# Kernel optimization log

Hardware: AMD Instinct MI355X
Metric: run time of the kernel (lower is better)

Reference implementation:

```python
import jax, jax.numpy as jnp
import numpy as np

NUM_LANDMARKS = 256
PINV_ITERS = 6


def iterative_inv(K):
    # Newton-Schulz iterative pseudo-inverse (Nystromformer), K: [B, m, m]
    I = jnp.eye(K.shape[-1], dtype=K.dtype)
    V = K.swapaxes(-1, -2) / (jnp.max(jnp.sum(K, axis=-2)) * jnp.max(jnp.sum(K, axis=-1)))
    for _ in range(PINV_ITERS):
        KV = K @ V
        V = 0.25 * V @ (13.0 * I - KV @ (15.0 * I - KV @ (7.0 * I - KV)))
    return V


def nystrom_attention_matrix(q, k, m):
    # q, k: [B, N, d] -> approximate softmax(q k^T / sqrt(d)) of shape [B, N, N]
    B, N, d = q.shape
    scale = 1.0 / jnp.sqrt(jnp.asarray(d, q.dtype))
    L = N // m
    q_l = q.reshape(B, m, L, d).mean(axis=2)  # landmark queries [B, m, d]
    k_l = k.reshape(B, m, L, d).mean(axis=2)  # landmark keys    [B, m, d]
    k1 = jax.nn.softmax(jnp.einsum('bnd,bmd->bnm', q, k_l) * scale, axis=-1)   # [B, N, m]
    k2 = jax.nn.softmax(jnp.einsum('bld,bmd->blm', q_l, k_l) * scale, axis=-1) # [B, m, m]
    k3 = jax.nn.softmax(jnp.einsum('bmd,bnd->bmn', q_l, k) * scale, axis=-1)   # [B, m, N]
    return (k1 @ iterative_inv(k2)) @ k3  # [B, N, N]


def setup_inputs() -> dict:
    key = jax.random.key(0)
    ks = jax.random.split(key, 8)
    B, C, T, W, H = 2, 64, 4, 32, 32
    d = C // 8
    scale = 0.05  # keep q.k scores in a sane softmax range
    return {
        'x': jax.random.normal(ks[0], (B, C, T, W, H), dtype=jnp.float32),
        'wq': jax.random.normal(ks[1], (d, C), dtype=jnp.float32) * scale,
        'bq': jax.random.normal(ks[2], (d,), dtype=jnp.float32) * scale,
        'wk': jax.random.normal(ks[3], (d, C), dtype=jnp.float32) * scale,
        'bk': jax.random.normal(ks[4], (d,), dtype=jnp.float32) * scale,
        'wv': jax.random.normal(ks[5], (C, C), dtype=jnp.float32) * scale,
        'bv': jax.random.normal(ks[6], (C,), dtype=jnp.float32) * scale,
        'gamma': jax.random.normal(ks[7], (1,), dtype=jnp.float32),
    }


def reference(x, wq, bq, wk, bk, wv, bv, gamma):
    B, C, T, W, H = x.shape
    N = T * W * H
    xf = x.reshape(B, C, N)
    # 1x1x1 Conv3d == per-token linear over channels
    q = jnp.einsum('oc,bcn->bno', wq, xf) + bq            # [B, N, C//8]
    k = jnp.einsum('oc,bcn->bno', wk, xf) + bk            # [B, N, C//8]
    v = jnp.einsum('oc,bcn->bon', wv, xf) + bv[None, :, None]  # [B, C, N]
    attn = nystrom_attention_matrix(q, k, NUM_LANDMARKS)  # [B, N, N]
    # out = bmm(value, attn^T): out[b,c,i] = sum_j v[b,c,j] * attn[b,i,j]
    out = jnp.einsum('bcj,bij->bci', v, attn).reshape(B, C, T, W, H)
    out = gamma[0] * out + x
    return out, attn
```

## Files before the change

### kernel.cpp

```cpp
#include <hip/hip_runtime.h>
#include <hip/hip_bf16.h>
#include <math.h>

#define NB 2
#define NC 64
#define ND 8
#define NN 4096
#define NM 256
#define NL 16
#define SCALE 0.35355339059327373f

typedef __attribute__((ext_vector_type(4))) float f32x4;
typedef __attribute__((ext_vector_type(8))) short bf16x8;

__device__ inline ushort f2bf(float f) {
  __hip_bfloat16 h = __float2bfloat16(f);
  return *reinterpret_cast<ushort*>(&h);
}
__device__ inline float bf2f(ushort u) {
  return __uint_as_float(((unsigned int)u) << 16);
}

__device__ inline void gl_lds16(const void* g, void* l) {
  __builtin_amdgcn_global_load_lds(
      (const __attribute__((address_space(1))) unsigned int*)g,
      (__attribute__((address_space(3))) unsigned int*)l, 16, 0, 0);
}

__global__ __launch_bounds__(256) void qkv2_kernel(
    const float* __restrict__ x,
    const float* __restrict__ wq, const float* __restrict__ bq,
    const float* __restrict__ wk, const float* __restrict__ bk,
    const float* __restrict__ wv, const float* __restrict__ bv,
    float* __restrict__ q, float* __restrict__ k, float* __restrict__ v) {
  __shared__ float ws[NC];
  int o = blockIdx.x;
  int b = blockIdx.z;
  int n0 = blockIdx.y * 1024;
  int t = threadIdx.x;
  const float* wrow;
  float bias;
  if (o < ND)            { wrow = wq + (size_t)o * NC;            bias = bq[o]; }
  else if (o < 2 * ND)   { wrow = wk + (size_t)(o - ND) * NC;     bias = bk[o - ND]; }
  else                   { wrow = wv + (size_t)(o - 2 * ND) * NC; bias = bv[o - 2 * ND]; }
  if (t < NC) ws[t] = wrow[t];
  __syncthreads();
  int n = n0 + t * 4;
  float4 acc = {bias, bias, bias, bias};
  #pragma unroll
  for (int c = 0; c < NC; ++c) {
    float wc = ws[c];
    float4 xv = *(const float4*)(x + ((size_t)b * NC + c) * NN + n);
    acc.x += wc * xv.x; acc.y += wc * xv.y; acc.z += wc * xv.z; acc.w += wc * xv.w;
  }
  if (o < ND) {
    float* qp = q + ((size_t)b * NN + n) * ND + o;
    qp[0] = acc.x; qp[8] = acc.y; qp[16] = acc.z; qp[24] = acc.w;
  } else if (o < 2 * ND) {
    float* kp = k + ((size_t)b * NN + n) * ND + (o - ND);
    kp[0] = acc.x; kp[8] = acc.y; kp[16] = acc.z; kp[24] = acc.w;
  } else {
    *(float4*)(v + ((size_t)b * NC + (o - 2 * ND)) * NN + n) = acc;
  }
}

__global__ void landmark_kernel(const float* __restrict__ q, const float* __restrict__ k,
                                float* __restrict__ ql, float* __restrict__ kl) {
  int idx = blockIdx.x * 256 + threadIdx.x;
  int b = idx / (NM * ND), r = idx % (NM * ND), i = r / ND, o = r % ND;
  float sq = 0.f, sk = 0.f;
  for (int l = 0; l < NL; ++l) {
    size_t base = ((size_t)b * NN + i * NL + l) * ND + o;
    sq += q[base]; sk += k[base];
  }
  ql[idx] = sq * (1.0f / NL);
  kl[idx] = sk * (1.0f / NL);
}

__global__ __launch_bounds__(256) void scores_softmax_m_bf16(
    const float* __restrict__ Q, int R, const float* __restrict__ KL,
    ushort* __restrict__ out) {
  __shared__ float skl[NM][9];
  int b = blockIdx.y;
  int t = threadIdx.x;
  for (int i = t; i < NM * ND; i += 256) skl[i >> 3][i & 7] = KL[(size_t)b * NM * ND + i];
  __syncthreads();
  int wave = t >> 6, lane = t & 63;
  int r = blockIdx.x * 4 + wave;
  const float* qrow = Q + ((size_t)b * R + r) * ND;
  float qr[ND];
  #pragma unroll
  for (int dd = 0; dd < ND; ++dd) qr[dd] = qrow[dd];
  float sc[4];
  float lmax = -1e30f;
  #pragma unroll
  for (int s = 0; s < 4; ++s) {
    int j = lane + 64 * s;
    float a = 0.f;
    #pragma unroll
    for (int dd = 0; dd < ND; ++dd) a += qr[dd] * skl[j][dd];
    sc[s] = a * SCALE;
    lmax = fmaxf(lmax, sc[s]);
  }
  for (int off = 32; off; off >>= 1) lmax = fmaxf(lmax, __shfl_xor(lmax, off));
  float lsum = 0.f;
  #pragma unroll
  for (int s = 0; s < 4; ++s) { sc[s] = expf(sc[s] - lmax); lsum += sc[s]; }
  for (int off = 32; off; off >>= 1) lsum += __shfl_xor(lsum, off);
  float inv = 1.0f / lsum;
  #pragma unroll
  for (int s = 0; s < 4; ++s)
    out[((size_t)b * R + r) * NM + lane + 64 * s] = f2bf(sc[s] * inv);
}

__global__ __launch_bounds__(256) void scores_softmax_m_f32(
    const float* __restrict__ Q, int R, const float* __restrict__ KL,
    float* __restrict__ out) {
  __shared__ float skl[NM][9];
  int b = blockIdx.y;
  int t = threadIdx.x;
  for (int i = t; i < NM * ND; i += 256) skl[i >> 3][i & 7] = KL[(size_t)b * NM * ND + i];
  __syncthreads();
  int wave = t >> 6, lane = t & 63;
  int r = blockIdx.x * 4 + wave;
  const float* qrow = Q + ((size_t)b * R + r) * ND;
  float qr[ND];
  #pragma unroll
  for (int dd = 0; dd < ND; ++dd) qr[dd] = qrow[dd];
  float sc[4];
  float lmax = -1e30f;
  #pragma unroll
  for (int s = 0; s < 4; ++s) {
    int j = lane + 64 * s;
    float a = 0.f;
    #pragma unroll
    for (int dd = 0; dd < ND; ++dd) a += qr[dd] * skl[j][dd];
    sc[s] = a * SCALE;
    lmax = fmaxf(lmax, sc[s]);
  }
  for (int off = 32; off; off >>= 1) lmax = fmaxf(lmax, __shfl_xor(lmax, off));
  float lsum = 0.f;
  #pragma unroll
  for (int s = 0; s < 4; ++s) { sc[s] = expf(sc[s] - lmax); lsum += sc[s]; }
  for (int off = 32; off; off >>= 1) lsum += __shfl_xor(lsum, off);
  float inv = 1.0f / lsum;
  #pragma unroll
  for (int s = 0; s < 4; ++s) out[((size_t)b * R + r) * NM + lane + 64 * s] = sc[s] * inv;
}

__global__ __launch_bounds__(256) void scores_softmax_n(
    const float* __restrict__ QL, const float* __restrict__ Kt,
    float* __restrict__ out) {
  __shared__ float wred[4], wsum[4];
  int b = blockIdx.y, i = blockIdx.x;
  int t = threadIdx.x;
  float qr[ND];
  #pragma unroll
  for (int dd = 0; dd < ND; ++dd) qr[dd] = QL[((size_t)b * NM + i) * ND + dd];
  float sc[16];
  float lmax = -1e30f;
  #pragma unroll
  for (int s = 0; s < 16; ++s) {
    int n = t + 256 * s;
    const float* kp = Kt + ((size_t)b * NN + n) * ND;
    float a = 0.f;
    #pragma unroll
    for (int dd = 0; dd < ND; ++dd) a += qr[dd] * kp[dd];
    sc[s] = a * SCALE;
    lmax = fmaxf(lmax, sc[s]);
  }
  for (int off = 32; off; off >>= 1) lmax = fmaxf(lmax, __shfl_xor(lmax, off));
  if ((t & 63) == 0) wred[t >> 6] = lmax;
  __syncthreads();
  lmax = fmaxf(fmaxf(wred[0], wred[1]), fmaxf(wred[2], wred[3]));
  float lsum = 0.f;
  #pragma unroll
  for (int s = 0; s < 16; ++s) { sc[s] = expf(sc[s] - lmax); lsum += sc[s]; }
  for (int off = 32; off; off >>= 1) lsum += __shfl_xor(lsum, off);
  if ((t & 63) == 0) wsum[t >> 6] = lsum;
  __syncthreads();
  lsum = wsum[0] + wsum[1] + wsum[2] + wsum[3];
  float inv = 1.0f / lsum;
  #pragma unroll
  for (int s = 0; s < 16; ++s) out[((size_t)b * NM + i) * NN + t + 256 * s] = sc[s] * inv;
}

__global__ __launch_bounds__(256) void denom_kernel(const float* __restrict__ k2,
                                                    float* __restrict__ denw) {
  __shared__ float red[256];
  int b = blockIdx.x;
  int t = threadIdx.x;
  float cs = 0.f;
  for (int i = 0; i < NM; ++i) cs += k2[((size_t)b * NM + i) * NM + t];
  red[t] = cs;
  __syncthreads();
  for (int off = 128; off; off >>= 1) {
    if (t < off) red[t] = fmaxf(red[t], red[t + off]);
    __syncthreads();
  }
  if (t == 0) denw[b] = red[0];
}

__global__ void vinit_kernel(const float* __restrict__ k2, const float* __restrict__ denw,
                             float* __restrict__ V) {
  int idx = blockIdx.x * 256 + threadIdx.x;
  int b = idx / (NM * NM), r = idx % (NM * NM), i = r / NM, j = r % NM;
  float dval = 1.0f / fmaxf(denw[0], denw[1]);
  V[idx] = k2[((size_t)b * NM + j) * NM + i] * dval;
}

__global__ __launch_bounds__(256) void gemm_rk32(
    const float* __restrict__ A, const float* __restrict__ Bm,
    float* __restrict__ out, float s_a, float s_ab) {
  int b = blockIdx.z;
  int bi = blockIdx.y * 32, bj = blockIdx.x * 32;
  __shared__ float As[32][260];
  __shared__ float Bs[256][36];
  int t = threadIdx.x;
  const float* Ab = A + (size_t)b * NM * NM;
  const float* Bb = Bm + (size_t)b * NM * NM;
  #pragma unroll
  for (int q = 0; q < 8; ++q) {
    int s = q * 256 + t;
    int ar = s >> 6, ac = (s & 63) * 4;
    *(float4*)&As[ar][ac] = *(const float4*)(Ab + (size_t)(bi + ar) * NM + ac);
    int br = s >> 3, bc = (s & 7) * 4;
    *(float4*)&Bs[br][bc] = *(const float4*)(Bb + (size_t)br * NM + bj + bc);
  }
  __syncthreads();
  int tx = t & 15, ty = t >> 4;
  float acc[2][2] = {};
  #pragma unroll 8
  for (int kk = 0; kk < NM; ++kk) {
    float a0 = As[ty * 2][kk], a1 = As[ty * 2 + 1][kk];
    float b0 = Bs[kk][tx * 2], b1 = Bs[kk][tx * 2 + 1];
    acc[0][0] += a0 * b0; acc[0][1] += a0 * b1;
    acc[1][0] += a1 * b0; acc[1][1] += a1 * b1;
  }
  #pragma unroll
  for (int i = 0; i < 2; ++i)
    #pragma unroll
    for (int j = 0; j < 2; ++j) {
      size_t o = ((size_t)b * NM + bi + ty * 2 + i) * NM + bj + tx * 2 + j;
      float r = s_ab * acc[i][j];
      if (s_a != 0.0f) r += s_a * A[o];
      out[o] = r;
    }
}

__global__ __launch_bounds__(256) void cvt_vinv_kernel(const float* __restrict__ Va,
                                                       ushort* __restrict__ Vt) {
  int b = blockIdx.z;
  int n0 = blockIdx.x * 32, m0 = blockIdx.y * 32;
  __shared__ float tile[32][33];
  int t = threadIdx.x;
  int r = t >> 3, c4 = (t & 7) * 4;
  float4 v = *(const float4*)(Va + ((size_t)b * NM + m0 + r) * NM + n0 + c4);
  tile[c4][r] = v.x; tile[c4 + 1][r] = v.y; tile[c4 + 2][r] = v.z; tile[c4 + 3][r] = v.w;
  __syncthreads();
  ushort4 u;
  u.x = f2bf(tile[r][c4]);     u.y = f2bf(tile[r][c4 + 1]);
  u.z = f2bf(tile[r][c4 + 2]); u.w = f2bf(tile[r][c4 + 3]);
  *(ushort4*)(Vt + ((size_t)b * NM + n0 + r) * NM + m0 + c4) = u;
}

__global__ __launch_bounds__(256) void cvt_t_kernel(const float* __restrict__ k3,
                                                    ushort* __restrict__ k3t) {
  int b = blockIdx.z;
  int n0 = blockIdx.x * 32, m0 = blockIdx.y * 32;
  __shared__ float tile[32][33];
  int t = threadIdx.x;
  int r = t >> 3, c4 = (t & 7) * 4;
  float4 v = *(const float4*)(k3 + ((size_t)b * NM + m0 + r) * NN + n0 + c4);
  tile[c4][r] = v.x; tile[c4 + 1][r] = v.y; tile[c4 + 2][r] = v.z; tile[c4 + 3][r] = v.w;
  __syncthreads();
  ushort4 u;
  u.x = f2bf(tile[r][c4]);     u.y = f2bf(tile[r][c4 + 1]);
  u.z = f2bf(tile[r][c4 + 2]); u.w = f2bf(tile[r][c4 + 3]);
  *(ushort4*)(k3t + ((size_t)b * NN + n0 + r) * NM + m0 + c4) = u;
}

__global__ __launch_bounds__(256) void gemm_a_mfma(
    const ushort* __restrict__ k1bf, const ushort* __restrict__ Vt,
    ushort* __restrict__ Abf) {
  int b = blockIdx.z;
  int bi = blockIdx.y * 128, bj = blockIdx.x * 128;
  __shared__ ushort As[128 * 64];
  __shared__ ushort Bs[128 * 64];
  int t = threadIdx.x;
  int wave = t >> 6, lane = t & 63;
  int wr = wave >> 1, wc = wave & 1;
  const ushort* Ab = k1bf + (size_t)b * NN * NM;
  const ushort* Bb = Vt + (size_t)b * NM * NM;
  f32x4 acc[4][4] = {};
  for (int k0 = 0; k0 < NM; k0 += 64) {
    #pragma unroll
    for (int q = 0; q < 4; ++q) {
      int s = q * 256 + t;
      int r = s >> 3, c = s & 7;
      int cs = (c ^ (r & 7)) << 3;
      gl_lds16(Ab + (size_t)(bi + r) * NM + k0 + cs, As + (size_t)s * 8);
      gl_lds16(Bb + (size_t)(bj + r) * NM + k0 + cs, Bs + (size_t)s * 8);
    }
    __syncthreads();
    #pragma unroll
    for (int kk = 0; kk < 2; ++kk) {
      int koff = kk * 64 + (lane >> 4) * 16;
      bf16x8 af[4], bfv[4];
      #pragma unroll
      for (int mi = 0; mi < 4; ++mi) {
        int row = wr * 64 + mi * 16 + (lane & 15);
        af[mi] = *(const bf16x8*)((const char*)As + row * 128 + (koff ^ ((row & 7) << 4)));
      }
      #pragma unroll
      for (int nj = 0; nj < 4; ++nj) {
        int row = wc * 64 + nj * 16 + (lane & 15);
        bfv[nj] = *(const bf16x8*)((const char*)Bs + row * 128 + (koff ^ ((row & 7) << 4)));
      }
      #pragma unroll
      for (int mi = 0; mi < 4; ++mi)
        #pragma unroll
        for (int nj = 0; nj < 4; ++nj)
          acc[mi][nj] = __builtin_amdgcn_mfma_f32_16x16x32_bf16(af[mi], bfv[nj], acc[mi][nj], 0, 0, 0);
    }
    __syncthreads();
  }
  int col = lane & 15, rbase = (lane >> 4) * 4;
  #pragma unroll
  for (int mi = 0; mi < 4; ++mi)
    #pragma unroll
    for (int nj = 0; nj < 4; ++nj)
      #pragma unroll
      for (int r = 0; r < 4; ++r)
        Abf[((size_t)b * NN + bi + wr * 64 + mi * 16 + rbase + r) * NM
            + bj + wc * 64 + nj * 16 + col] = f2bf(acc[mi][nj][r]);
}

__global__ __launch_bounds__(256) void gemm_attn_mfma(
    const ushort* __restrict__ Abf, const ushort* __restrict__ K3T,
    float* __restrict__ attn) {
  int lin = blockIdx.z * 1024 + blockIdx.y * 32 + blockIdx.x;
  int swz = (lin & 7) * 256 + (lin >> 3);
  int b = swz >> 10;
  int rem = swz & 1023;
  int bi = (rem >> 5) * 128, bj = (rem & 31) * 128;
  __shared__ ushort As[128 * 64];
  __shared__ ushort Bs[128 * 64];
  int t = threadIdx.x;
  int wave = t >> 6, lane = t & 63;
  int wr = wave >> 1, wc = wave & 1;
  const ushort* Ab = Abf + (size_t)b * NN * NM;
  const ushort* Bb = K3T + (size_t)b * NN * NM;
  f32x4 acc[4][4] = {};
  for (int k0 = 0; k0 < NM; k0 += 64) {
    #pragma unroll
    for (int q = 0; q < 4; ++q) {
      int s = q * 256 + t;
      int r = s >> 3, c = s & 7;
      int cs = (c ^ (r & 7)) << 3;
      gl_lds16(Ab + (size_t)(bi + r) * NM + k0 + cs, As + (size_t)s * 8);
      gl_lds16(Bb + (size_t)(bj + r) * NM + k0 + cs, Bs + (size_t)s * 8);
    }
    __syncthreads();
    #pragma unroll
    for (int kk = 0; kk < 2; ++kk) {
      int koff = kk * 64 + (lane >> 4) * 16;
      bf16x8 af[4], bfv[4];
      #pragma unroll
      for (int mi = 0; mi < 4; ++mi) {
        int row = wr * 64 + mi * 16 + (lane & 15);
        af[mi] = *(const bf16x8*)((const char*)As + row * 128 + (koff ^ ((row & 7) << 4)));
      }
      #pragma unroll
      for (int nj = 0; nj < 4; ++nj) {
        int row = wc * 64 + nj * 16 + (lane & 15);
        bfv[nj] = *(const bf16x8*)((const char*)Bs + row * 128 + (koff ^ ((row & 7) << 4)));
      }
      #pragma unroll
      for (int mi = 0; mi < 4; ++mi)
        #pragma unroll
        for (int nj = 0; nj < 4; ++nj)
          acc[mi][nj] = __builtin_amdgcn_mfma_f32_16x16x32_bf16(af[mi], bfv[nj], acc[mi][nj], 0, 0, 0);
    }
    __syncthreads();
  }
  int col = lane & 15, rbase = (lane >> 4) * 4;
  #pragma unroll
  for (int mi = 0; mi < 4; ++mi)
    #pragma unroll
    for (int nj = 0; nj < 4; ++nj)
      #pragma unroll
      for (int r = 0; r < 4; ++r)
        attn[((size_t)b * NN + bi + wr * 64 + mi * 16 + rbase + r) * NN
             + bj + wc * 64 + nj * 16 + col] = acc[mi][nj][r];
}

__global__ __launch_bounds__(256) void kv_kernel(
    const float* __restrict__ K3, const float* __restrict__ Vv,
    float* __restrict__ kvout) {
  int b = blockIdx.z, bp = blockIdx.x * 64;
  int j0base = blockIdx.y * (NN / 32);
  __shared__ float Ks[64][33], Vs[64][33];
  int t = threadIdx.x, tx = t & 15, ty = t >> 4;
  int lrow = t >> 2, ljc = (t & 3) * 8;
  float acc[4][4] = {};
  for (int j0 = j0base; j0 < j0base + NN / 32; j0 += 32) {
    float4 a0 = *(const float4*)(K3 + ((size_t)b * NM + bp + lrow) * NN + j0 + ljc);
    float4 a1 = *(const float4*)(K3 + ((size_t)b * NM + bp + lrow) * NN + j0 + ljc + 4);
    float4 v0 = *(const float4*)(Vv + ((size_t)b * NC + lrow) * NN + j0 + ljc);
    float4 v1 = *(const float4*)(Vv + ((size_t)b * NC + lrow) * NN + j0 + ljc + 4);
    Ks[lrow][ljc + 0] = a0.x; Ks[lrow][ljc + 1] = a0.y; Ks[lrow][ljc + 2] = a0.z; Ks[lrow][ljc + 3] = a0.w;
    Ks[lrow][ljc + 4] = a1.x; Ks[lrow][ljc + 5] = a1.y; Ks[lrow][ljc + 6] = a1.z; Ks[lrow][ljc + 7] = a1.w;
    Vs[lrow][ljc + 0] = v0.x; Vs[lrow][ljc + 1] = v0.y; Vs[lrow][ljc + 2] = v0.z; Vs[lrow][ljc + 3] = v0.w;
    Vs[lrow][ljc + 4] = v1.x; Vs[lrow][ljc + 5] = v1.y; Vs[lrow][ljc + 6] = v1.z; Vs[lrow][ljc + 7] = v1.w;
    __syncthreads();
    #pragma unroll
    for (int kk = 0; kk < 32; ++kk) {
      float av_[4], bv_[4];
      #pragma unroll
      for (int i = 0; i < 4; ++i) av_[i] = Ks[(ty << 2) + i][kk];
      #pragma unroll
      for (int j = 0; j < 4; ++j) bv_[j] = Vs[(tx << 2) + j][kk];
      #pragma unroll
      for (int i = 0; i < 4; ++i)
        #pragma unroll
        for (int j = 0; j < 4; ++j) acc[i][j] += av_[i] * bv_[j];
    }
    __syncthreads();
  }
  #pragma unroll
  for (int i = 0; i < 4; ++i)
    #pragma unroll
    for (int j = 0; j < 4; ++j)
      atomicAdd(&kvout[((size_t)b * NM + bp + (ty << 2) + i) * NC + (tx << 2) + j], acc[i][j]);
}

__global__ __launch_bounds__(256) void out_kernel(
    const ushort* __restrict__ Abf, const float* __restrict__ kvm,
    const float* __restrict__ x, const float* __restrict__ gamma,
    float* __restrict__ outp) {
  __shared__ float As[32 * 256];
  int blk = blockIdx.x;
  int b = blk / (NN / 32), n0 = (blk % (NN / 32)) * 32;
  int t = threadIdx.x;
  for (int it = 0; it < 32; ++it)
    As[it * 256 + (t ^ (it & 31))] = bf2f(Abf[((size_t)b * NN + n0 + it) * NM + t]);
  __syncthreads();
  int tn = t & 31, cg0 = (t >> 5) * 8;
  float g = gamma[0];
  float acc[8] = {};
  for (int p = 0; p < NM; ++p) {
    float a = As[tn * 256 + (p ^ (tn & 31))];
    float4 kv0 = *(const float4*)(kvm + ((size_t)b * NM + p) * NC + cg0);
    float4 kv1 = *(const float4*)(kvm + ((size_t)b * NM + p) * NC + cg0 + 4);
    acc[0] += a * kv0.x; acc[1] += a * kv0.y; acc[2] += a * kv0.z; acc[3] += a * kv0.w;
    acc[4] += a * kv1.x; acc[5] += a * kv1.y; acc[6] += a * kv1.z; acc[7] += a * kv1.w;
  }
  #pragma unroll
  for (int qd = 0; qd < 8; ++qd) {
    int c = cg0 + qd;
    size_t idx = ((size_t)b * NC + c) * NN + n0 + tn;
    outp[idx] = g * acc[qd] + x[idx];
  }
}

extern "C" void kernel_launch(void* const* d_in, const int* in_sizes, int n_in,
                              void* d_out, int out_size, void* d_ws, size_t ws_size,
                              hipStream_t stream) {
  const float* x     = (const float*)d_in[0];
  const float* wq    = (const float*)d_in[1];
  const float* bq    = (const float*)d_in[2];
  const float* wk    = (const float*)d_in[3];
  const float* bk    = (const float*)d_in[4];
  const float* wv    = (const float*)d_in[5];
  const float* bv    = (const float*)d_in[6];
  const float* gamma = (const float*)d_in[7];
  float* outp = (float*)d_out;
  float* attn = outp + (size_t)NB * NC * NN;
  float* w = (float*)d_ws;

  float* qw   = w;
  float* kw   = qw + 65536;
  float* vw   = kw + 65536;
  float* qlw  = vw + 524288;
  float* klw  = qlw + 4096;
  float* k1w  = klw + 4096;
  float* k2w  = k1w + 2097152;
  float* k3w  = k2w + 131072;
  float* Abuf = k3w + 2097152;
  float* Va   = Abuf + 2097152;
  float* Vb   = Va + 131072;
  float* Zb   = Vb + 131072;
  float* T1   = Zb + 131072;
  float* T2   = T1 + 131072;
  float* kvw  = T2 + 131072;
  float* denw = kvw + 32768;
  ushort* k1bf  = (ushort*)k1w;
  ushort* k3T   = (ushort*)k1w + 2097152;
  ushort* Abf   = (ushort*)Abuf;
  ushort* Vinvt = (ushort*)Zb;

  hipMemsetAsync(kvw, 0, (size_t)NB * NM * NC * sizeof(float), stream);
  qkv2_kernel<<<dim3(80, NN / 1024, NB), dim3(256), 0, stream>>>(
      x, wq, bq, wk, bk, wv, bv, qw, kw, vw);
  landmark_kernel<<<dim3(NB * NM * ND / 256), dim3(256), 0, stream>>>(qw, kw, qlw, klw);
  scores_softmax_m_bf16<<<dim3(NN / 4, NB), dim3(256), 0, stream>>>(qw, NN, klw, k1bf);
  scores_softmax_m_f32<<<dim3(NM / 4, NB), dim3(256), 0, stream>>>(qlw, NM, klw, k2w);
  scores_softmax_n<<<dim3(NM, NB), dim3(256), 0, stream>>>(qlw, kw, k3w);
  denom_kernel<<<dim3(NB), dim3(256), 0, stream>>>(k2w, denw);
  vinit_kernel<<<dim3(NB * NM * NM / 256), dim3(256), 0, stream>>>(k2w, denw, Va);

  float* Vc = Va; float* Vn = Vb;
  for (int it = 0; it < 6; ++it) {
    gemm_rk32<<<dim3(8, 8, NB), dim3(256), 0, stream>>>(k2w, Vc, Zb, 0.f, 1.f);
    gemm_rk32<<<dim3(8, 8, NB), dim3(256), 0, stream>>>(Zb, Zb, T1, 7.f, -1.f);
    gemm_rk32<<<dim3(8, 8, NB), dim3(256), 0, stream>>>(Zb, T1, T2, 15.f, -1.f);
    gemm_rk32<<<dim3(8, 8, NB), dim3(256), 0, stream>>>(Vc, T2, Vn, 3.25f, -0.25f);
    float* tmp = Vc; Vc = Vn; Vn = tmp;
  }

  cvt_vinv_kernel<<<dim3(NM / 32, NM / 32, NB), dim3(256), 0, stream>>>(Va, Vinvt);
  cvt_t_kernel<<<dim3(NN / 32, NM / 32, NB), dim3(256), 0, stream>>>(k3w, k3T);
  gemm_a_mfma<<<dim3(NM / 128, NN / 128, NB), dim3(256), 0, stream>>>(k1bf, Vinvt, Abf);
  gemm_attn_mfma<<<dim3(NN / 128, NN / 128, NB), dim3(256), 0, stream>>>(Abf, k3T, attn);
  kv_kernel<<<dim3(NM / 64, 32, NB), dim3(256), 0, stream>>>(k3w, vw, kvw);
  out_kernel<<<dim3(NB * NN / 32), dim3(256), 0, stream>>>(Abf, kvw, x, gamma, outp);
}
```

Baseline: 303.2 us.

## Factor Newton-Schulz polynomial into three GEMMs and pad launches with independent work

Each Newton-Schulz iteration is rewritten from four dependent 256x256 GEMMs into three launches. It factors the cubic polynomial into a linear root term and a quadratic, so U=VZ−aV and Z² run in one launch, and the quadratic plus identity is folded into the B-tile load of the final GEMM. The idle CUs in these 128-block launches are filled with the k3 transpose/bf16 conversion and the k3·v reduction, which are spread across the 18 launches. The standalone cvt_t and kv kernels are removed. This cuts the launch count and serial dependency depth, at the cost of a numerically different but algebraically equivalent polynomial evaluation with irrational coefficients.

```diff
diff --git a/kernel.cpp b/kernel.cpp
--- a/kernel.cpp
+++ b/kernel.cpp
@@ -9,6 +9,9 @@
 #define NM 256
 #define NL 16
 #define SCALE 0.35355339059327373f
+#define A_ROOT 4.1303956f
+#define B_COEF (-2.8696044f)
+#define C_COEF 3.1474086f
 
 typedef __attribute__((ext_vector_type(4))) float f32x4;
 typedef __attribute__((ext_vector_type(8))) short bf16x8;
@@ -209,23 +212,93 @@
   V[idx] = k2[((size_t)b * NM + j) * NM + i] * dval;
 }
 
-__global__ __launch_bounds__(256) void gemm_rk32(
-    const float* __restrict__ A, const float* __restrict__ Bm,
-    float* __restrict__ out, float s_a, float s_ab) {
-  int b = blockIdx.z;
-  int bi = blockIdx.y * 32, bj = blockIdx.x * 32;
-  __shared__ float As[32][260];
-  __shared__ float Bs[256][36];
-  int t = threadIdx.x;
-  const float* Ab = A + (size_t)b * NM * NM;
-  const float* Bb = Bm + (size_t)b * NM * NM;
+#define NS_SMEM 70144
+
+__device__ __forceinline__ void pad_work(
+    int p, const float* __restrict__ k3, ushort* __restrict__ k3t,
+    const float* __restrict__ vw, float* __restrict__ kvw, char* smem, int t) {
+  if (p < 2048) {
+    typedef float TRow[33];
+    TRow* tile = (TRow*)smem;
+    int n0 = (p & 127) * 32, m0 = ((p >> 7) & 7) * 32, b = p >> 10;
+    int rr = t >> 3, c4 = (t & 7) * 4;
+    float4 v = *(const float4*)(k3 + ((size_t)b * NM + m0 + rr) * NN + n0 + c4);
+    tile[c4][rr] = v.x; tile[c4 + 1][rr] = v.y; tile[c4 + 2][rr] = v.z; tile[c4 + 3][rr] = v.w;
+    __syncthreads();
+    ushort4 u;
+    u.x = f2bf(tile[rr][c4]);     u.y = f2bf(tile[rr][c4 + 1]);
+    u.z = f2bf(tile[rr][c4 + 2]); u.w = f2bf(tile[rr][c4 + 3]);
+    *(ushort4*)(k3t + ((size_t)b * NN + n0 + rr) * NM + m0 + c4) = u;
+  } else {
+    typedef float KVRow[33];
+    KVRow* Ks = (KVRow*)smem;
+    KVRow* Vs = (KVRow*)(smem + 64 * 33 * 4);
+    int p2 = p - 2048;
+    int bp = (p2 & 3) * 64;
+    int jsl = (p2 >> 2) & 31;
+    int b = p2 >> 7;
+    int j0base = jsl * (NN / 32);
+    int tx = t & 15, ty = t >> 4;
+    int lrow = t >> 2, ljc = (t & 3) * 8;
+    float acc[4][4] = {};
+    for (int j0 = j0base; j0 < j0base + NN / 32; j0 += 32) {
+      float4 a0 = *(const float4*)(k3 + ((size_t)b * NM + bp + lrow) * NN + j0 + ljc);
+      float4 a1 = *(const float4*)(k3 + ((size_t)b * NM + bp + lrow) * NN + j0 + ljc + 4);
+      float4 v0 = *(const float4*)(vw + ((size_t)b * NC + lrow) * NN + j0 + ljc);
+      float4 v1 = *(const float4*)(vw + ((size_t)b * NC + lrow) * NN + j0 + ljc + 4);
+      Ks[lrow][ljc + 0] = a0.x; Ks[lrow][ljc + 1] = a0.y; Ks[lrow][ljc + 2] = a0.z; Ks[lrow][ljc + 3] = a0.w;
+      Ks[lrow][ljc + 4] = a1.x; Ks[lrow][ljc + 5] = a1.y; Ks[lrow][ljc + 6] = a1.z; Ks[lrow][ljc + 7] = a1.w;
+      Vs[lrow][ljc + 0] = v0.x; Vs[lrow][ljc + 1] = v0.y; Vs[lrow][ljc + 2] = v0.z; Vs[lrow][ljc + 3] = v0.w;
+      Vs[lrow][ljc + 4] = v1.x; Vs[lrow][ljc + 5] = v1.y; Vs[lrow][ljc + 6] = v1.z; Vs[lrow][ljc + 7] = v1.w;
+      __syncthreads();
+      #pragma unroll
+      for (int kk = 0; kk < 32; ++kk) {
+        float av_[4], bv_[4];
+        #pragma unroll
+        for (int i = 0; i < 4; ++i) av_[i] = Ks[(ty << 2) + i][kk];
+        #pragma unroll
+        for (int j = 0; j < 4; ++j) bv_[j] = Vs[(tx << 2) + j][kk];
+        #pragma unroll
+        for (int i = 0; i < 4; ++i)
+          #pragma unroll
+          for (int j = 0; j < 4; ++j) acc[i][j] += av_[i] * bv_[j];
+      }
+      __syncthreads();
+    }
+    #pragma unroll
+    for (int i = 0; i < 4; ++i)
+      #pragma unroll
+      for (int j = 0; j < 4; ++j)
+        atomicAdd(&kvw[((size_t)b * NM + bp + (ty << 2) + i) * NC + (tx << 2) + j], acc[i][j]);
+  }
+}
+
+__device__ __forceinline__ void ns_tile(
+    const float* __restrict__ A, const float* __restrict__ B,
+    const float* __restrict__ B2, float* __restrict__ O,
+    float s_a, float s_ab, size_t bo, int bi, int bj, char* smem, int t) {
+  typedef float ARow[260];
+  typedef float BRow[36];
+  ARow* As = (ARow*)smem;
+  BRow* Bs = (BRow*)(smem + 33280);
   #pragma unroll
   for (int q = 0; q < 8; ++q) {
     int s = q * 256 + t;
     int ar = s >> 6, ac = (s & 63) * 4;
-    *(float4*)&As[ar][ac] = *(const float4*)(Ab + (size_t)(bi + ar) * NM + ac);
-    int br = s >> 3, bc = (s & 7) * 4;
-    *(float4*)&Bs[br][bc] = *(const float4*)(Bb + (size_t)br * NM + bj + bc);
+    *(float4*)&As[ar][ac] = *(const float4*)(A + bo + (size_t)(bi + ar) * NM + ac);
+    int bk = s >> 3, bc = (s & 7) * 4;
+    if (B2 == nullptr) {
+      *(float4*)&Bs[bk][bc] = *(const float4*)(B + bo + (size_t)bk * NM + bj + bc);
+    } else {
+      float4 v = *(const float4*)(B + bo + (size_t)bk * NM + bj + bc);
+      float4 z = *(const float4*)(B2 + bo + (size_t)bk * NM + bj + bc);
+      float4 rr;
+      rr.x = v.x + B_COEF * z.x; rr.y = v.y + B_COEF * z.y;
+      rr.z = v.z + B_COEF * z.z; rr.w = v.w + B_COEF * z.w;
+      int d = bk - bj - bc;
+      if (d >= 0 && d < 4) ((float*)&rr)[d] += C_COEF;
+      *(float4*)&Bs[bk][bc] = rr;
+    }
   }
   __syncthreads();
   int tx = t & 15, ty = t >> 4;
@@ -241,11 +314,63 @@
   for (int i = 0; i < 2; ++i)
     #pragma unroll
     for (int j = 0; j < 2; ++j) {
-      size_t o = ((size_t)b * NM + bi + ty * 2 + i) * NM + bj + tx * 2 + j;
+      size_t o = bo + (size_t)(bi + ty * 2 + i) * NM + bj + tx * 2 + j;
       float r = s_ab * acc[i][j];
       if (s_a != 0.0f) r += s_a * A[o];
-      out[o] = r;
-    }
+      O[o] = r;
+    }
+}
+
+__global__ __launch_bounds__(256) void ns_z_kernel(
+    const float* __restrict__ k2, const float* __restrict__ V, float* __restrict__ Z,
+    const float* __restrict__ k3, ushort* __restrict__ k3t,
+    const float* __restrict__ vw, float* __restrict__ kvw, int padBase) {
+  __shared__ char smem[NS_SMEM];
+  int blk = blockIdx.x, t = threadIdx.x;
+  if (blk < NB * 64) {
+    int b = blk >> 6, tile = blk & 63;
+    int bi = (tile >> 3) * 32, bj = (tile & 7) * 32;
+    ns_tile(k2, V, nullptr, Z, 0.f, 1.f, (size_t)b * NM * NM, bi, bj, smem, t);
+  } else {
+    pad_work(padBase + blk - NB * 64, k3, k3t, vw, kvw, smem, t);
+  }
+}
+
+__global__ __launch_bounds__(256) void ns_uz2_kernel(
+    const float* __restrict__ V, const float* __restrict__ Z,
+    float* __restrict__ U, float* __restrict__ Z2,
+    const float* __restrict__ k3, ushort* __restrict__ k3t,
+    const float* __restrict__ vw, float* __restrict__ kvw, int padBase) {
+  __shared__ char smem[NS_SMEM];
+  int blk = blockIdx.x, t = threadIdx.x;
+  if (blk < NB * 64) {
+    int b = blk >> 6, tile = blk & 63;
+    int bi = (tile >> 3) * 32, bj = (tile & 7) * 32;
+    ns_tile(V, Z, nullptr, U, -A_ROOT, 1.f, (size_t)b * NM * NM, bi, bj, smem, t);
+  } else if (blk < 2 * NB * 64) {
+    int r = blk - NB * 64;
+    int b = r >> 6, tile = r & 63;
+    int bi = (tile >> 3) * 32, bj = (tile & 7) * 32;
+    ns_tile(Z, Z, nullptr, Z2, 0.f, 1.f, (size_t)b * NM * NM, bi, bj, smem, t);
+  } else {
+    pad_work(padBase + blk - 2 * NB * 64, k3, k3t, vw, kvw, smem, t);
+  }
+}
+
+__global__ __launch_bounds__(256) void ns_v_kernel(
+    const float* __restrict__ U, const float* __restrict__ Z2,
+    const float* __restrict__ Z, float* __restrict__ Vout,
+    const float* __restrict__ k3, ushort* __restrict__ k3t,
+    const float* __restrict__ vw, float* __restrict__ kvw, int padBase) {
+  __shared__ char smem[NS_SMEM];
+  int blk = blockIdx.x, t = threadIdx.x;
+  if (blk < NB * 64) {
+    int b = blk >> 6, tile = blk & 63;
+    int bi = (tile >> 3) * 32, bj = (tile & 7) * 32;
+    ns_tile(U, Z2, Z, Vout, 0.f, -0.25f, (size_t)b * NM * NM, bi, bj, smem, t);
+  } else {
+    pad_work(padBase + blk - NB * 64, k3, k3t, vw, kvw, smem, t);
+  }
 }
 
 __global__ __launch_bounds__(256) void cvt_vinv_kernel(const float* __restrict__ Va,
@@ -262,22 +387,6 @@
   u.x = f2bf(tile[r][c4]);     u.y = f2bf(tile[r][c4 + 1]);
   u.z = f2bf(tile[r][c4 + 2]); u.w = f2bf(tile[r][c4 + 3]);
   *(ushort4*)(Vt + ((size_t)b * NM + n0 + r) * NM + m0 + c4) = u;
-}
-
-__global__ __launch_bounds__(256) void cvt_t_kernel(const float* __restrict__ k3,
-                                                    ushort* __restrict__ k3t) {
-  int b = blockIdx.z;
-  int n0 = blockIdx.x * 32, m0 = blockIdx.y * 32;
-  __shared__ float tile[32][33];
-  int t = threadIdx.x;
-  int r = t >> 3, c4 = (t & 7) * 4;
-  float4 v = *(const float4*)(k3 + ((size_t)b * NM + m0 + r) * NN + n0 + c4);
-  tile[c4][r] = v.x; tile[c4 + 1][r] = v.y; tile[c4 + 2][r] = v.z; tile[c4 + 3][r] = v.w;
-  __syncthreads();
-  ushort4 u;
-  u.x = f2bf(tile[r][c4]);     u.y = f2bf(tile[r][c4 + 1]);
-  u.z = f2bf(tile[r][c4 + 2]); u.w = f2bf(tile[r][c4 + 3]);
-  *(ushort4*)(k3t + ((size_t)b * NN + n0 + r) * NM + m0 + c4) = u;
 }
 
 __global__ __launch_bounds__(256) void gemm_a_mfma(
@@ -393,47 +502,7 @@
       for (int r = 0; r < 4; ++r)
         attn[((size_t)b * NN + bi + wr * 64 + mi * 16 + rbase + r) * NN
              + bj + wc * 64 + nj * 16 + col] = acc[mi][nj][r];
-}
-
-__global__ __launch_bounds__(256) void kv_kernel(
-    const float* __restrict__ K3, const float* __restrict__ Vv,
-    float* __restrict__ kvout) {
-  int b = blockIdx.z, bp = blockIdx.x * 64;
-  int j0base = blockIdx.y * (NN / 32);
-  __shared__ float Ks[64][33], Vs[64][33];
-  int t = threadIdx.x, tx = t & 15, ty = t >> 4;
-  int lrow = t >> 2, ljc = (t & 3) * 8;
-  float acc[4][4] = {};
-  for (int j0 = j0base; j0 < j0base + NN / 32; j0 += 32) {
-    float4 a0 = *(const float4*)(K3 + ((size_t)b * NM + bp + lrow) * NN + j0 + ljc);
-    float4 a1 = *(const float4*)(K3 + ((size_t)b * NM + bp + lrow) * NN + j0 + ljc + 4);
-    float4 v0 = *(const float4*)(Vv + ((size_t)b * NC + lrow) * NN + j0 + ljc);
-    float4 v1 = *(const float4*)(Vv + ((size_t)b * NC + lrow) * NN + j0 + ljc + 4);
-    Ks[lrow][ljc + 0] = a0.x; Ks[lrow][ljc + 1] = a0.y; Ks[lrow][ljc + 2] = a0.z; Ks[lrow][ljc + 3] = a0.w;
-    Ks[lrow][ljc + 4] = a1.x; Ks[lrow][ljc + 5] = a1.y; Ks[lrow][ljc + 6] = a1.z; Ks[lrow][ljc + 7] = a1.w;
-    Vs[lrow][ljc + 0] = v0.x; Vs[lrow][ljc + 1] = v0.y; Vs[lrow][ljc + 2] = v0.z; Vs[lrow][ljc + 3] = v0.w;
-    Vs[lrow][ljc + 4] = v1.x; Vs[lrow][ljc + 5] = v1.y; Vs[lrow][ljc + 6] = v1.z; Vs[lrow][ljc + 7] = v1.w;
-    __syncthreads();
-    #pragma unroll
-    for (int kk = 0; kk < 32; ++kk) {
-      float av_[4], bv_[4];
-      #pragma unroll
-      for (int i = 0; i < 4; ++i) av_[i] = Ks[(ty << 2) + i][kk];
-      #pragma unroll
-      for (int j = 0; j < 4; ++j) bv_[j] = Vs[(tx << 2) + j][kk];
-      #pragma unroll
-      for (int i = 0; i < 4; ++i)
-        #pragma unroll
-        for (int j = 0; j < 4; ++j) acc[i][j] += av_[i] * bv_[j];
-    }
-    __syncthreads();
-  }
-  #pragma unroll
-  for (int i = 0; i < 4; ++i)
-    #pragma unroll
-    for (int j = 0; j < 4; ++j)
-      atomicAdd(&kvout[((size_t)b * NM + bp + (ty << 2) + i) * NC + (tx << 2) + j], acc[i][j]);
-}
+  }
 
 __global__ __launch_bounds__(256) void out_kernel(
     const ushort* __restrict__ Abf, const float* __restrict__ kvm,
@@ -488,17 +557,17 @@
   float* k2w  = k1w + 2097152;
   float* k3w  = k2w + 131072;
   float* Abuf = k3w + 2097152;
-  float* Va   = Abuf + 2097152;
-  float* Vb   = Va + 131072;
-  float* Zb   = Vb + 131072;
-  float* T1   = Zb + 131072;
-  float* T2   = T1 + 131072;
-  float* kvw  = T2 + 131072;
+  float* Zb   = Abuf + 1048576;
+  float* Z2b  = Zb + 131072;
+  float* Ub   = Z2b + 131072;
+  float* Va   = Ub + 131072;
+  float* Vtw  = Va + 131072;
+  float* kvw  = Vtw + 65536;
   float* denw = kvw + 32768;
   ushort* k1bf  = (ushort*)k1w;
   ushort* k3T   = (ushort*)k1w + 2097152;
   ushort* Abf   = (ushort*)Abuf;
-  ushort* Vinvt = (ushort*)Zb;
+  ushort* Vinvt = (ushort*)Vtw;
 
   hipMemsetAsync(kvw, 0, (size_t)NB * NM * NC * sizeof(float), stream);
   qkv2_kernel<<<dim3(80, NN / 1024, NB), dim3(256), 0, stream>>>(
@@ -510,19 +579,21 @@
   denom_kernel<<<dim3(NB), dim3(256), 0, stream>>>(k2w, denw);
   vinit_kernel<<<dim3(NB * NM * NM / 256), dim3(256), 0, stream>>>(k2w, denw, Va);
 
-  float* Vc = Va; float* Vn = Vb;
+  int padBase = 0;
   for (int it = 0; it < 6; ++it) {
-    gemm_rk32<<<dim3(8, 8, NB), dim3(256), 0, stream>>>(k2w, Vc, Zb, 0.f, 1.f);
-    gemm_rk32<<<dim3(8, 8, NB), dim3(256), 0, stream>>>(Zb, Zb, T1, 7.f, -1.f);
-    gemm_rk32<<<dim3(8, 8, NB), dim3(256), 0, stream>>>(Zb, T1, T2, 15.f, -1.f);
-    gemm_rk32<<<dim3(8, 8, NB), dim3(256), 0, stream>>>(Vc, T2, Vn, 3.25f, -0.25f);
-    float* tmp = Vc; Vc = Vn; Vn = tmp;
+    ns_z_kernel<<<dim3(NB * 64 + 128), dim3(256), 0, stream>>>(
+        k2w, Va, Zb, k3w, k3T, vw, kvw, padBase);
+    padBase += 128;
+    ns_uz2_kernel<<<dim3(2 * NB * 64 + 128), dim3(256), 0, stream>>>(
+        Va, Zb, Ub, Z2b, k3w, k3T, vw, kvw, padBase);
+    padBase += 128;
+    ns_v_kernel<<<dim3(NB * 64 + 128), dim3(256), 0, stream>>>(
+        Ub, Z2b, Zb, Va, k3w, k3T, vw, kvw, padBase);
+    padBase += 128;
   }
 
   cvt_vinv_kernel<<<dim3(NM / 32, NM / 32, NB), dim3(256), 0, stream>>>(Va, Vinvt);
-  cvt_t_kernel<<<dim3(NN / 32, NM / 32, NB), dim3(256), 0, stream>>>(k3w, k3T);
   gemm_a_mfma<<<dim3(NM / 128, NN / 128, NB), dim3(256), 0, stream>>>(k1bf, Vinvt, Abf);
   gemm_attn_mfma<<<dim3(NN / 128, NN / 128, NB), dim3(256), 0, stream>>>(Abf, k3T, attn);
-  kv_kernel<<<dim3(NM / 64, 32, NB), dim3(256), 0, stream>>>(k3w, vw, kvw);
   out_kernel<<<dim3(NB * NN / 32), dim3(256), 0, stream>>>(Abf, kvw, x, gamma, outp);
 }
```

New measurement: 312.4 us. +3.0%, slower.

## Fuse landmark pooling into QKV projection and merge softmax score kernels

Applied to the files above, without the earlier changes.

The landmark averaging is folded into the QKV projection kernel with a 4-lane shuffle reduction, and the three score/softmax kernels are merged into one launch that dispatches on block index. This removes several launches and the extra pass over q/k. Nontemporal stores are used for the large attn and output writes to avoid cache pollution. Workspace layout is adjusted and the inverse source is now Vc rather than Va, which is the same buffer after six swaps.

```diff
diff --git a/kernel.cpp b/kernel.cpp
--- a/kernel.cpp
+++ b/kernel.cpp
@@ -27,12 +27,13 @@
       (__attribute__((address_space(3))) unsigned int*)l, 16, 0, 0);
 }
 
-__global__ __launch_bounds__(256) void qkv2_kernel(
+__global__ __launch_bounds__(256) void qkv2l_kernel(
     const float* __restrict__ x,
     const float* __restrict__ wq, const float* __restrict__ bq,
     const float* __restrict__ wk, const float* __restrict__ bk,
     const float* __restrict__ wv, const float* __restrict__ bv,
-    float* __restrict__ q, float* __restrict__ k, float* __restrict__ v) {
+    float* __restrict__ q, float* __restrict__ k, float* __restrict__ v,
+    float* __restrict__ ql, float* __restrict__ kl) {
   __shared__ float ws[NC];
   int o = blockIdx.x;
   int b = blockIdx.z;
@@ -62,127 +63,99 @@
   } else {
     *(float4*)(v + ((size_t)b * NC + (o - 2 * ND)) * NN + n) = acc;
   }
-}
-
-__global__ void landmark_kernel(const float* __restrict__ q, const float* __restrict__ k,
-                                float* __restrict__ ql, float* __restrict__ kl) {
-  int idx = blockIdx.x * 256 + threadIdx.x;
-  int b = idx / (NM * ND), r = idx % (NM * ND), i = r / ND, o = r % ND;
-  float sq = 0.f, sk = 0.f;
-  for (int l = 0; l < NL; ++l) {
-    size_t base = ((size_t)b * NN + i * NL + l) * ND + o;
-    sq += q[base]; sk += k[base];
-  }
-  ql[idx] = sq * (1.0f / NL);
-  kl[idx] = sk * (1.0f / NL);
-}
-
-__global__ __launch_bounds__(256) void scores_softmax_m_bf16(
-    const float* __restrict__ Q, int R, const float* __restrict__ KL,
-    ushort* __restrict__ out) {
+  if (o < 2 * ND) {
+    float s4 = acc.x + acc.y + acc.z + acc.w;
+    s4 += __shfl_xor(s4, 1);
+    s4 += __shfl_xor(s4, 2);
+    if ((t & 3) == 0) {
+      int g = n0 / 16 + (t >> 2);
+      float* dst = (o < ND) ? ql : kl;
+      dst[((size_t)b * NM + g) * ND + (o & 7)] = s4 * (1.0f / 16.0f);
+    }
+  }
+}
+
+__global__ __launch_bounds__(256) void scores_all_kernel(
+    const float* __restrict__ q, const float* __restrict__ ql,
+    const float* __restrict__ kw, const float* __restrict__ kl,
+    ushort* __restrict__ k1bf, float* __restrict__ k2w,
+    float* __restrict__ k3w) {
   __shared__ float skl[NM][9];
-  int b = blockIdx.y;
-  int t = threadIdx.x;
-  for (int i = t; i < NM * ND; i += 256) skl[i >> 3][i & 7] = KL[(size_t)b * NM * ND + i];
-  __syncthreads();
-  int wave = t >> 6, lane = t & 63;
-  int r = blockIdx.x * 4 + wave;
-  const float* qrow = Q + ((size_t)b * R + r) * ND;
-  float qr[ND];
-  #pragma unroll
-  for (int dd = 0; dd < ND; ++dd) qr[dd] = qrow[dd];
-  float sc[4];
-  float lmax = -1e30f;
-  #pragma unroll
-  for (int s = 0; s < 4; ++s) {
-    int j = lane + 64 * s;
-    float a = 0.f;
-    #pragma unroll
-    for (int dd = 0; dd < ND; ++dd) a += qr[dd] * skl[j][dd];
-    sc[s] = a * SCALE;
-    lmax = fmaxf(lmax, sc[s]);
-  }
-  for (int off = 32; off; off >>= 1) lmax = fmaxf(lmax, __shfl_xor(lmax, off));
-  float lsum = 0.f;
-  #pragma unroll
-  for (int s = 0; s < 4; ++s) { sc[s] = expf(sc[s] - lmax); lsum += sc[s]; }
-  for (int off = 32; off; off >>= 1) lsum += __shfl_xor(lsum, off);
-  float inv = 1.0f / lsum;
-  #pragma unroll
-  for (int s = 0; s < 4; ++s)
-    out[((size_t)b * R + r) * NM + lane + 64 * s] = f2bf(sc[s] * inv);
-}
-
-__global__ __launch_bounds__(256) void scores_softmax_m_f32(
-    const float* __restrict__ Q, int R, const float* __restrict__ KL,
-    float* __restrict__ out) {
-  __shared__ float skl[NM][9];
-  int b = blockIdx.y;
-  int t = threadIdx.x;
-  for (int i = t; i < NM * ND; i += 256) skl[i >> 3][i & 7] = KL[(size_t)b * NM * ND + i];
-  __syncthreads();
-  int wave = t >> 6, lane = t & 63;
-  int r = blockIdx.x * 4 + wave;
-  const float* qrow = Q + ((size_t)b * R + r) * ND;
-  float qr[ND];
-  #pragma unroll
-  for (int dd = 0; dd < ND; ++dd) qr[dd] = qrow[dd];
-  float sc[4];
-  float lmax = -1e30f;
-  #pragma unroll
-  for (int s = 0; s < 4; ++s) {
-    int j = lane + 64 * s;
-    float a = 0.f;
-    #pragma unroll
-    for (int dd = 0; dd < ND; ++dd) a += qr[dd] * skl[j][dd];
-    sc[s] = a * SCALE;
-    lmax = fmaxf(lmax, sc[s]);
-  }
-  for (int off = 32; off; off >>= 1) lmax = fmaxf(lmax, __shfl_xor(lmax, off));
-  float lsum = 0.f;
-  #pragma unroll
-  for (int s = 0; s < 4; ++s) { sc[s] = expf(sc[s] - lmax); lsum += sc[s]; }
-  for (int off = 32; off; off >>= 1) lsum += __shfl_xor(lsum, off);
-  float inv = 1.0f / lsum;
-  #pragma unroll
-  for (int s = 0; s < 4; ++s) out[((size_t)b * R + r) * NM + lane + 64 * s] = sc[s] * inv;
-}
-
-__global__ __launch_bounds__(256) void scores_softmax_n(
-    const float* __restrict__ QL, const float* __restrict__ Kt,
-    float* __restrict__ out) {
   __shared__ float wred[4], wsum[4];
-  int b = blockIdx.y, i = blockIdx.x;
-  int t = threadIdx.x;
-  float qr[ND];
-  #pragma unroll
-  for (int dd = 0; dd < ND; ++dd) qr[dd] = QL[((size_t)b * NM + i) * ND + dd];
-  float sc[16];
-  float lmax = -1e30f;
-  #pragma unroll
-  for (int s = 0; s < 16; ++s) {
-    int n = t + 256 * s;
-    const float* kp = Kt + ((size_t)b * NN + n) * ND;
-    float a = 0.f;
-    #pragma unroll
-    for (int dd = 0; dd < ND; ++dd) a += qr[dd] * kp[dd];
-    sc[s] = a * SCALE;
-    lmax = fmaxf(lmax, sc[s]);
-  }
-  for (int off = 32; off; off >>= 1) lmax = fmaxf(lmax, __shfl_xor(lmax, off));
-  if ((t & 63) == 0) wred[t >> 6] = lmax;
-  __syncthreads();
-  lmax = fmaxf(fmaxf(wred[0], wred[1]), fmaxf(wred[2], wred[3]));
-  float lsum = 0.f;
-  #pragma unroll
-  for (int s = 0; s < 16; ++s) { sc[s] = expf(sc[s] - lmax); lsum += sc[s]; }
-  for (int off = 32; off; off >>= 1) lsum += __shfl_xor(lsum, off);
-  if ((t & 63) == 0) wsum[t >> 6] = lsum;
-  __syncthreads();
-  lsum = wsum[0] + wsum[1] + wsum[2] + wsum[3];
-  float inv = 1.0f / lsum;
-  #pragma unroll
-  for (int s = 0; s < 16; ++s) out[((size_t)b * NM + i) * NN + t + 256 * s] = sc[s] * inv;
+  int blk = blockIdx.x;
+  int t = threadIdx.x;
+  if (blk < 2048 + 128) {
+    const float* Q; int R, b, xrow;
+    bool isbf;
+    if (blk < 2048) { b = blk >> 10; xrow = blk & 1023; Q = q;  R = NN; isbf = true; }
+    else { int r = blk - 2048; b = r >> 6; xrow = r & 63; Q = ql; R = NM; isbf = false; }
+    for (int i = t; i < NM * ND; i += 256) skl[i >> 3][i & 7] = kl[(size_t)b * NM * ND + i];
+    __syncthreads();
+    int wave = t >> 6, lane = t & 63;
+    int r = xrow * 4 + wave;
+    const float* qrow = Q + ((size_t)b * R + r) * ND;
+    float qr[ND];
+    #pragma unroll
+    for (int dd = 0; dd < ND; ++dd) qr[dd] = qrow[dd];
+    float sc[4];
+    float lmax = -1e30f;
+    #pragma unroll
+    for (int s = 0; s < 4; ++s) {
+      int j = lane + 64 * s;
+      float a = 0.f;
+      #pragma unroll
+      for (int dd = 0; dd < ND; ++dd) a += qr[dd] * skl[j][dd];
+      sc[s] = a * SCALE;
+      lmax = fmaxf(lmax, sc[s]);
+    }
+    for (int off = 32; off; off >>= 1) lmax = fmaxf(lmax, __shfl_xor(lmax, off));
+    float lsum = 0.f;
+    #pragma unroll
+    for (int s = 0; s < 4; ++s) { sc[s] = expf(sc[s] - lmax); lsum += sc[s]; }
+    for (int off = 32; off; off >>= 1) lsum += __shfl_xor(lsum, off);
+    float inv = 1.0f / lsum;
+    if (isbf) {
+      #pragma unroll
+      for (int s = 0; s < 4; ++s)
+        k1bf[((size_t)b * R + r) * NM + lane + 64 * s] = f2bf(sc[s] * inv);
+    } else {
+      #pragma unroll
+      for (int s = 0; s < 4; ++s)
+        k2w[((size_t)b * R + r) * NM + lane + 64 * s] = sc[s] * inv;
+    }
+  } else {
+    int r = blk - 2176;
+    int b = r >> 8, i = r & 255;
+    float qr[ND];
+    #pragma unroll
+    for (int dd = 0; dd < ND; ++dd) qr[dd] = ql[((size_t)b * NM + i) * ND + dd];
+    float sc[16];
+    float lmax = -1e30f;
+    #pragma unroll
+    for (int s = 0; s < 16; ++s) {
+      int n = t + 256 * s;
+      const float* kp = kw + ((size_t)b * NN + n) * ND;
+      float a = 0.f;
+      #pragma unroll
+      for (int dd = 0; dd < ND; ++dd) a += qr[dd] * kp[dd];
+      sc[s] = a * SCALE;
+      lmax = fmaxf(lmax, sc[s]);
+    }
+    for (int off = 32; off; off >>= 1) lmax = fmaxf(lmax, __shfl_xor(lmax, off));
+    if ((t & 63) == 0) wred[t >> 6] = lmax;
+    __syncthreads();
+    lmax = fmaxf(fmaxf(wred[0], wred[1]), fmaxf(wred[2], wred[3]));
+    float lsum = 0.f;
+    #pragma unroll
+    for (int s = 0; s < 16; ++s) { sc[s] = expf(sc[s] - lmax); lsum += sc[s]; }
+    for (int off = 32; off; off >>= 1) lsum += __shfl_xor(lsum, off);
+    if ((t & 63) == 0) wsum[t >> 6] = lsum;
+    __syncthreads();
+    lsum = wsum[0] + wsum[1] + wsum[2] + wsum[3];
+    float inv = 1.0f / lsum;
+    #pragma unroll
+    for (int s = 0; s < 16; ++s) k3w[((size_t)b * NM + i) * NN + t + 256 * s] = sc[s] * inv;
+  }
 }
 
 __global__ __launch_bounds__(256) void denom_kernel(const float* __restrict__ k2,
@@ -391,8 +364,10 @@
     for (int nj = 0; nj < 4; ++nj)
       #pragma unroll
       for (int r = 0; r < 4; ++r)
-        attn[((size_t)b * NN + bi + wr * 64 + mi * 16 + rbase + r) * NN
-             + bj + wc * 64 + nj * 16 + col] = acc[mi][nj][r];
+        __builtin_nontemporal_store(
+            acc[mi][nj][r],
+            &attn[((size_t)b * NN + bi + wr * 64 + mi * 16 + rbase + r) * NN
+                  + bj + wc * 64 + nj * 16 + col]);
 }
 
 __global__ __launch_bounds__(256) void kv_kernel(
@@ -460,7 +435,7 @@
   for (int qd = 0; qd < 8; ++qd) {
     int c = cg0 + qd;
     size_t idx = ((size_t)b * NC + c) * NN + n0 + tn;
-    outp[idx] = g * acc[qd] + x[idx];
+    __builtin_nontemporal_store(g * acc[qd] + x[idx], &outp[idx]);
   }
 }
 
@@ -488,25 +463,24 @@
   float* k2w  = k1w + 2097152;
   float* k3w  = k2w + 131072;
   float* Abuf = k3w + 2097152;
-  float* Va   = Abuf + 2097152;
+  float* Va   = Abuf + 1048576;
   float* Vb   = Va + 131072;
   float* Zb   = Vb + 131072;
   float* T1   = Zb + 131072;
   float* T2   = T1 + 131072;
-  float* kvw  = T2 + 131072;
+  float* Vtw  = T2 + 131072;
+  float* kvw  = Vtw + 65536;
   float* denw = kvw + 32768;
   ushort* k1bf  = (ushort*)k1w;
   ushort* k3T   = (ushort*)k1w + 2097152;
   ushort* Abf   = (ushort*)Abuf;
-  ushort* Vinvt = (ushort*)Zb;
+  ushort* Vinvt = (ushort*)Vtw;
 
   hipMemsetAsync(kvw, 0, (size_t)NB * NM * NC * sizeof(float), stream);
-  qkv2_kernel<<<dim3(80, NN / 1024, NB), dim3(256), 0, stream>>>(
-      x, wq, bq, wk, bk, wv, bv, qw, kw, vw);
-  landmark_kernel<<<dim3(NB * NM * ND / 256), dim3(256), 0, stream>>>(qw, kw, qlw, klw);
-  scores_softmax_m_bf16<<<dim3(NN / 4, NB), dim3(256), 0, stream>>>(qw, NN, klw, k1bf);
-  scores_softmax_m_f32<<<dim3(NM / 4, NB), dim3(256), 0, stream>>>(qlw, NM, klw, k2w);
-  scores_softmax_n<<<dim3(NM, NB), dim3(256), 0, stream>>>(qlw, kw, k3w);
+  qkv2l_kernel<<<dim3(80, NN / 1024, NB), dim3(256), 0, stream>>>(
+      x, wq, bq, wk, bk, wv, bv, qw, kw, vw, qlw, klw);
+  scores_all_kernel<<<dim3(2048 + 128 + 512), dim3(256), 0, stream>>>(
+      qw, qlw, kw, klw, k1bf, k2w, k3w);
   denom_kernel<<<dim3(NB), dim3(256), 0, stream>>>(k2w, denw);
   vinit_kernel<<<dim3(NB * NM * NM / 256), dim3(256), 0, stream>>>(k2w, denw, Va);
 
@@ -519,7 +493,7 @@
     float* tmp = Vc; Vc = Vn; Vn = tmp;
   }
 
-  cvt_vinv_kernel<<<dim3(NM / 32, NM / 32, NB), dim3(256), 0, stream>>>(Va, Vinvt);
+  cvt_vinv_kernel<<<dim3(NM / 32, NM / 32, NB), dim3(256), 0, stream>>>(Vc, Vinvt);
   cvt_t_kernel<<<dim3(NN / 32, NM / 32, NB), dim3(256), 0, stream>>>(k3w, k3T);
   gemm_a_mfma<<<dim3(NM / 128, NN / 128, NB), dim3(256), 0, stream>>>(k1bf, Vinvt, Abf);
   gemm_attn_mfma<<<dim3(NN / 128, NN / 128, NB), dim3(256), 0, stream>>>(Abf, k3T, attn);
```

Measured after the change: 302.0 us. About the same (-0.4%).
